# Performance work log

Hardware: AMD Instinct MI355X
Metric: run time of the kernel (lower is better)

The kernel has to match this reference:

```python
import jax, jax.numpy as jnp
import numpy as np

EPS = 1e-5

def _layer_norm(x, g, b):
    mu = jnp.mean(x, axis=-1, keepdims=True)
    var = jnp.mean(jnp.square(x - mu), axis=-1, keepdims=True)
    return (x - mu) * jax.lax.rsqrt(var + EPS) * g + b

def setup_inputs() -> dict:
    key = jax.random.key(0)
    ks = jax.random.split(key, 8)
    B, N, M = 4, 2048, 2048
    Dq, Dc = 512, 768
    H, Dh = 8, 64
    inner = H * Dh  # 512
    s = lambda d: 1.0 / np.sqrt(d)
    return {
        "x": jax.random.normal(ks[0], (B, N, Dq), jnp.float32),
        "cond": jax.random.normal(ks[1], (B, M, Dc), jnp.float32),
        "lnx_g": jnp.ones((Dq,), jnp.float32),
        "lnx_b": jnp.zeros((Dq,), jnp.float32),
        "lnc_g": jnp.ones((Dc,), jnp.float32),
        "lnc_b": jnp.zeros((Dc,), jnp.float32),
        "Wq": jax.random.normal(ks[2], (Dq, inner), jnp.float32) * s(Dq),
        "Wk": jax.random.normal(ks[3], (Dc, inner), jnp.float32) * s(Dc),
        "Wv": jax.random.normal(ks[4], (Dc, inner), jnp.float32) * s(Dc),
        "Wo": jax.random.normal(ks[5], (inner, Dq), jnp.float32) * s(inner),
        "bo": jnp.zeros((Dq,), jnp.float32),
        "lnf_g": jnp.ones((Dq,), jnp.float32),
        "lnf_b": jnp.zeros((Dq,), jnp.float32),
    }

def reference(x, cond, lnx_g, lnx_b, lnc_g, lnc_b, Wq, Wk, Wv, Wo, bo, lnf_g, lnf_b):
    H = 8
    B, N, _ = x.shape
    M = cond.shape[1]
    x_orig = x
    xn = _layer_norm(x, lnx_g, lnx_b)
    cn = _layer_norm(cond, lnc_g, lnc_b)
    q = (xn @ Wq).reshape(B, N, H, -1).transpose(0, 2, 1, 3)  # b h n d
    k = (cn @ Wk).reshape(B, M, H, -1).transpose(0, 2, 1, 3)  # b h m d
    v = (cn @ Wv).reshape(B, M, H, -1).transpose(0, 2, 1, 3)
    scale = q.shape[-1] ** -0.5
    sim = jnp.einsum('bhid,bhjd->bhij', q, k) * scale
    attn = jax.nn.softmax(sim, axis=-1)
    out = jnp.einsum('bhij,bhjd->bhid', attn, v)
    out = out.transpose(0, 2, 1, 3).reshape(B, N, -1)  # b n (h d)
    out = out @ Wo + bo
    out = out + x_orig  # residual=True
    return _layer_norm(out, lnf_g, lnf_b)
```

## Files before the change

### kernel.cpp

```cpp
#include <hip/hip_runtime.h>
#include <hip/hip_bf16.h>
#include <math.h>

#define BB 4
#define NN 2048
#define MM 2048
#define DQ 512
#define DC 768
#define NH 8
#define DH 64
#define INNER 512
#define KVS 1024

typedef short bf16x8 __attribute__((ext_vector_type(8)));
typedef float f32x4  __attribute__((ext_vector_type(4)));

__device__ inline short fbf(float f) {
    __hip_bfloat16 h = __float2bfloat16(f);
    return __builtin_bit_cast(short, h);
}

__device__ inline void gld16(const void* gptr, void* lds_uniform_base) {
    __builtin_amdgcn_global_load_lds(
        (const __attribute__((address_space(1))) void*)gptr,
        (__attribute__((address_space(3))) void*)lds_uniform_base, 16, 0, 0);
}

__global__ __launch_bounds__(256) void prep_k(
    const float* __restrict__ x, const float* __restrict__ cond,
    const float* __restrict__ gx, const float* __restrict__ bx_,
    const float* __restrict__ gc, const float* __restrict__ bc,
    short* __restrict__ xn, short* __restrict__ cn,
    const float* __restrict__ Wq, const float* __restrict__ Wk,
    const float* __restrict__ Wv, const float* __restrict__ Wo,
    short* __restrict__ Wqt, short* __restrict__ Wkvt, short* __restrict__ Wot)
{
    const int bxid = blockIdx.x;
    const int t = threadIdx.x;

    if (bxid < 16384) {
        const int which = bxid >> 13;
        const int row   = bxid & 8191;
        const float* in = which ? cond : x;
        const float* g  = which ? gc : gx;
        const float* bb = which ? bc : bx_;
        short* out      = which ? cn : xn;
        const int D     = which ? DC : DQ;

        const float* xr = in + (size_t)row * D;
        float s = 0.f, s2 = 0.f;
        for (int d = t; d < D; d += 256) {
            float v = xr[d];
            s += v; s2 += v * v;
        }
        __shared__ float red[2][4];
        #pragma unroll
        for (int off = 32; off; off >>= 1) {
            s  += __shfl_down(s,  off, 64);
            s2 += __shfl_down(s2, off, 64);
        }
        const int wave = t >> 6, lane = t & 63;
        if (lane == 0) { red[0][wave] = s; red[1][wave] = s2; }
        __syncthreads();
        if (t == 0) {
            float ts = red[0][0] + red[0][1] + red[0][2] + red[0][3];
            float t2 = red[1][0] + red[1][1] + red[1][2] + red[1][3];
            float mu = ts / (float)D;
            float var = t2 / (float)D - mu * mu;
            red[0][0] = mu;
            red[1][0] = rsqrtf(var + 1e-5f);
        }
        __syncthreads();
        const float mu = red[0][0], rstd = red[1][0];
        short* o = out + (size_t)row * D;
        for (int d = t; d < D; d += 256)
            o[d] = fbf((xr[d] - mu) * rstd * g[d] + bb[d]);
    } else {
        const int tb = bxid - 16384;
        const int y = tb >> 4;
        const int n0 = (tb & 15) * 32;
        const float* W; short* Wt; int K, k0;
        if (y < 16)      { W = Wq; Wt = Wqt;  K = DQ; k0 = y * 32; }
        else if (y < 40) { W = Wk; Wt = Wkvt; K = DC; k0 = (y - 16) * 32; }
        else if (y < 64) { W = Wv; Wt = Wkvt + (size_t)512 * DC; K = DC; k0 = (y - 40) * 32; }
        else             { W = Wo; Wt = Wot;  K = DQ; k0 = (y - 64) * 32; }

        __shared__ float tile[32][33];
        const int r = t >> 3, c4 = (t & 7) * 4;
        float4 vv = *(const float4*)&W[(size_t)(k0 + r) * 512 + n0 + c4];
        tile[c4 + 0][r] = vv.x; tile[c4 + 1][r] = vv.y;
        tile[c4 + 2][r] = vv.z; tile[c4 + 3][r] = vv.w;
        __syncthreads();
        short4 sv;
        sv.x = fbf(tile[r][c4 + 0]); sv.y = fbf(tile[r][c4 + 1]);
        sv.z = fbf(tile[r][c4 + 2]); sv.w = fbf(tile[r][c4 + 3]);
        *(short4*)&Wt[(size_t)(n0 + r) * K + k0 + c4] = sv;
    }
}

__global__ __launch_bounds__(256) void layernorm_res_f32(
    const short* __restrict__ ob, const float* __restrict__ x,
    const float* __restrict__ g, const float* __restrict__ b,
    float* __restrict__ out)
{
    const int row = blockIdx.x;
    const int t = threadIdx.x;
    const size_t base = (size_t)row * DQ;
    float v0, v1;
    {
        unsigned u0 = (unsigned)(unsigned short)ob[base + t];
        unsigned u1 = (unsigned)(unsigned short)ob[base + t + 256];
        v0 = __builtin_bit_cast(float, u0 << 16) + x[base + t];
        v1 = __builtin_bit_cast(float, u1 << 16) + x[base + t + 256];
    }
    float s = v0 + v1, s2 = v0 * v0 + v1 * v1;
    __shared__ float red[2][4];
    #pragma unroll
    for (int off = 32; off; off >>= 1) {
        s  += __shfl_down(s,  off, 64);
        s2 += __shfl_down(s2, off, 64);
    }
    const int wave = t >> 6, lane = t & 63;
    if (lane == 0) { red[0][wave] = s; red[1][wave] = s2; }
    __syncthreads();
    if (t == 0) {
        float ts = red[0][0] + red[0][1] + red[0][2] + red[0][3];
        float t2 = red[1][0] + red[1][1] + red[1][2] + red[1][3];
        float mu = ts / (float)DQ;
        float var = t2 / (float)DQ - mu * mu;
        red[0][0] = mu;
        red[1][0] = rsqrtf(var + 1e-5f);
    }
    __syncthreads();
    const float mu = red[0][0], rstd = red[1][0];
    out[base + t]       = (v0 - mu) * rstd * g[t]       + b[t];
    out[base + t + 256] = (v1 - mu) * rstd * g[t + 256] + b[t + 256];
}

#define GBK 32

__global__ __launch_bounds__(256) void qkv_gemm(
    const short* __restrict__ xn, const short* __restrict__ cn,
    const short* __restrict__ Wqt, const short* __restrict__ Wkvt,
    short* __restrict__ qb, short* __restrict__ kvb, float qsc)
{
    const short* A; const short* Bt; short* outp; int K, Nout, n0; float sc;
    if (blockIdx.x < 4) {
        A = xn; Bt = Wqt; outp = qb; K = DQ; Nout = 512;
        n0 = blockIdx.x * 128; sc = qsc;
    } else {
        A = cn; Bt = Wkvt; outp = kvb; K = DC; Nout = 1024;
        n0 = (blockIdx.x - 4) * 128; sc = 1.f;
    }
    __shared__ short As[128 * GBK];
    __shared__ short Bs[128 * GBK];
    const int t = threadIdx.x;
    const int w = t >> 6, lane = t & 63;
    const int quad = lane >> 4, l16 = lane & 15;
    const int m0 = blockIdx.y * 128;
    const int wm = (w >> 1) * 64, wn = (w & 1) * 64;

    f32x4 acc[4][4];
    #pragma unroll
    for (int i = 0; i < 4; ++i)
        #pragma unroll
        for (int j = 0; j < 4; ++j) acc[i][j] = (f32x4){0.f, 0.f, 0.f, 0.f};

    for (int kt = 0; kt < K; kt += GBK) {
        __syncthreads();
        #pragma unroll
        for (int i = 0; i < 2; ++i) {
            const int j = w * 2 + i;
            const int c = j * 64 + lane;
            gld16(&A[(size_t)(m0 + (c >> 2)) * K + kt + (c & 3) * 8],
                  (char*)As + j * 1024);
            gld16(&Bt[(size_t)(n0 + (c >> 2)) * K + kt + (c & 3) * 8],
                  (char*)Bs + j * 1024);
        }
        __syncthreads();

        bf16x8 af[4], bfr[4];
        #pragma unroll
        for (int mt = 0; mt < 4; ++mt)
            af[mt] = *(bf16x8*)&As[(wm + mt * 16 + l16) * GBK + quad * 8];
        #pragma unroll
        for (int nt = 0; nt < 4; ++nt)
            bfr[nt] = *(bf16x8*)&Bs[(wn + nt * 16 + l16) * GBK + quad * 8];
        #pragma unroll
        for (int mt = 0; mt < 4; ++mt)
            #pragma unroll
            for (int nt = 0; nt < 4; ++nt)
                acc[mt][nt] = __builtin_amdgcn_mfma_f32_16x16x32_bf16(
                    af[mt], bfr[nt], acc[mt][nt], 0, 0, 0);
    }

    #pragma unroll
    for (int mt = 0; mt < 4; ++mt)
        #pragma unroll
        for (int r = 0; r < 4; ++r) {
            const int m = m0 + wm + mt * 16 + quad * 4 + r;
            #pragma unroll
            for (int nt = 0; nt < 4; ++nt) {
                const int n = n0 + wn + nt * 16 + l16;
                outp[(size_t)m * Nout + n] = fbf(acc[mt][nt][r] * sc);
            }
        }
}

__global__ __launch_bounds__(256) void oproj_gemm(
    const short* __restrict__ A, const short* __restrict__ Bt,
    short* __restrict__ outb, const float* __restrict__ bias)
{
    const int K = INNER, Nout = INNER;
    __shared__ short As[128 * GBK];
    __shared__ short Bs[64 * GBK];
    const int t = threadIdx.x;
    const int w = t >> 6, lane = t & 63;
    const int quad = lane >> 4, l16 = lane & 15;
    const int m0 = blockIdx.y * 128, n0 = blockIdx.x * 64;
    const int wm = (w >> 1) * 64, wn = (w & 1) * 32;

    f32x4 acc[4][2];
    #pragma unroll
    for (int i = 0; i < 4; ++i)
        #pragma unroll
        for (int j = 0; j < 2; ++j) acc[i][j] = (f32x4){0.f, 0.f, 0.f, 0.f};

    for (int kt = 0; kt < K; kt += GBK) {
        __syncthreads();
        #pragma unroll
        for (int i = 0; i < 2; ++i) {
            const int j = w * 2 + i;
            const int c = j * 64 + lane;
            gld16(&A[(size_t)(m0 + (c >> 2)) * K + kt + (c & 3) * 8],
                  (char*)As + j * 1024);
        }
        {
            const int c = w * 64 + lane;
            gld16(&Bt[(size_t)(n0 + (c >> 2)) * K + kt + (c & 3) * 8],
                  (char*)Bs + w * 1024);
        }
        __syncthreads();

        bf16x8 af[4], bfr[2];
        #pragma unroll
        for (int mt = 0; mt < 4; ++mt)
            af[mt] = *(bf16x8*)&As[(wm + mt * 16 + l16) * GBK + quad * 8];
        #pragma unroll
        for (int nt = 0; nt < 2; ++nt)
            bfr[nt] = *(bf16x8*)&Bs[(wn + nt * 16 + l16) * GBK + quad * 8];
        #pragma unroll
        for (int mt = 0; mt < 4; ++mt)
            #pragma unroll
            for (int nt = 0; nt < 2; ++nt)
                acc[mt][nt] = __builtin_amdgcn_mfma_f32_16x16x32_bf16(
                    af[mt], bfr[nt], acc[mt][nt], 0, 0, 0);
    }

    #pragma unroll
    for (int mt = 0; mt < 4; ++mt)
        #pragma unroll
        for (int r = 0; r < 4; ++r) {
            const int m = m0 + wm + mt * 16 + quad * 4 + r;
            #pragma unroll
            for (int nt = 0; nt < 2; ++nt) {
                const int n = n0 + wn + nt * 16 + l16;
                outb[(size_t)m * Nout + n] = fbf(acc[mt][nt][r] + bias[n]);
            }
        }
}

#define QT 128
#define JT 64
#define KSTR 72
#define MH (MM / 2)
#define NIT (MH / JT)

__global__ __launch_bounds__(512) void attention_mfma(
    const short* __restrict__ q, const short* __restrict__ kv,
    short* __restrict__ o)
{
    const int b = blockIdx.z, h = blockIdx.y;
    const int i0 = blockIdx.x * QT;
    const int t = threadIdx.x;
    const int wave = t >> 6, lane = t & 63;
    const int w4 = wave & 3, hh = wave >> 2;
    const int quad = lane >> 4, l16 = lane & 15;

    __shared__ __align__(16) char smem[73728];
    typedef short KT[2][64][KSTR];
    KT* Ks = (KT*)smem;
    KT* Vt = (KT*)(smem + 36864);
    float (*Obuf)[32][68] = (float(*)[32][68])(smem);
    float (*Lbuf)[32]     = (float(*)[32])(smem + 34816);

    bf16x8 qf[2][2];
    #pragma unroll
    for (int it = 0; it < 2; ++it) {
        const int row = i0 + w4 * 32 + it * 16 + l16;
        const short* qp = &q[((size_t)(b * NN + row)) * INNER + h * DH];
        qf[it][0] = *(const bf16x8*)&qp[quad * 8];
        qf[it][1] = *(const bf16x8*)&qp[32 + quad * 8];
    }

    f32x4 Oa[2][4];
    f32x4 La[2];
    #pragma unroll
    for (int it = 0; it < 2; ++it) {
        La[it] = (f32x4){0.f, 0.f, 0.f, 0.f};
        #pragma unroll
        for (int dt = 0; dt < 4; ++dt) Oa[it][dt] = (f32x4){0.f, 0.f, 0.f, 0.f};
    }

    const bf16x8 ones8 = {(short)0x3F80, (short)0x3F80, (short)0x3F80, (short)0x3F80,
                          (short)0x3F80, (short)0x3F80, (short)0x3F80, (short)0x3F80};

    const int tt = t & 255, th = t >> 8;
    const int kjj = tt >> 3, kdq = (tt & 7) * 8;
    const int vjp = tt & 31, vd0 = (tt >> 5) * 8;

    const int jl0 = 2 * vjp;
    const int vcol = (jl0 >> 5) * 32 + (((jl0 >> 2) & 3) * 8)
                   + (((jl0 >> 4) & 1) * 4) + (jl0 & 3);

    const short* kp0 = kv + ((size_t)(b * MM + th * MH + kjj))      * KVS + h * DH + kdq;
    const short* kp1 = kv + ((size_t)(b * MM + th * MH + kjj + 32)) * KVS + h * DH + kdq;
    const short* vp0 = kv + ((size_t)(b * MM + th * MH + jl0))      * KVS + 512 + h * DH + vd0;
    const short* vp1 = vp0 + KVS;

    bf16x8 ka, kb2, va, vb;
    auto load = [&]() {
        ka  = *(const bf16x8*)kp0;
        kb2 = *(const bf16x8*)kp1;
        va  = *(const bf16x8*)vp0;
        vb  = *(const bf16x8*)vp1;
        kp0 += (size_t)JT * KVS; kp1 += (size_t)JT * KVS;
        vp0 += (size_t)JT * KVS; vp1 += (size_t)JT * KVS;
    };
    auto store = [&](int pb) {
        *(bf16x8*)&Ks[pb][th][kjj][kdq]      = ka;
        *(bf16x8*)&Ks[pb][th][kjj + 32][kdq] = kb2;
        #pragma unroll
        for (int i = 0; i < 8; ++i) {
            short2 pr; pr.x = va[i]; pr.y = vb[i];
            *(short2*)&Vt[pb][th][vd0 + i][vcol] = pr;
        }
    };

    load(); store(0);
    __syncthreads();

    for (int itr = 0; itr < NIT; ++itr) {
        const int p = itr & 1;
        const bool more = (itr + 1 < NIT);
        if (more) load();

        #pragma unroll
        for (int cc = 0; cc < 2; ++cc) {
            f32x4 Sc[2][2];
            #pragma unroll
            for (int jtl = 0; jtl < 2; ++jtl) {
                const int jt = cc * 2 + jtl;
                bf16x8 kf0 = *(bf16x8*)&Ks[p][hh][jt * 16 + l16][quad * 8];
                bf16x8 kf1 = *(bf16x8*)&Ks[p][hh][jt * 16 + l16][32 + quad * 8];
                #pragma unroll
                for (int it = 0; it < 2; ++it) {
                    f32x4 c = (f32x4){0.f, 0.f, 0.f, 0.f};
                    c = __builtin_amdgcn_mfma_f32_16x16x32_bf16(kf0, qf[it][0], c, 0, 0, 0);
                    c = __builtin_amdgcn_mfma_f32_16x16x32_bf16(kf1, qf[it][1], c, 0, 0, 0);
                    Sc[jtl][it] = c;
                }
            }

            bf16x8 p8[2];
            #pragma unroll
            for (int it = 0; it < 2; ++it) {
                const float e0 = exp2f(Sc[0][it][0]), e1 = exp2f(Sc[0][it][1]);
                const float e2 = exp2f(Sc[0][it][2]), e3 = exp2f(Sc[0][it][3]);
                const float f0 = exp2f(Sc[1][it][0]), f1 = exp2f(Sc[1][it][1]);
                const float f2 = exp2f(Sc[1][it][2]), f3 = exp2f(Sc[1][it][3]);
                uint4 pk;
                pk.x = __builtin_amdgcn_perm(__builtin_bit_cast(unsigned, e1),
                                             __builtin_bit_cast(unsigned, e0), 0x07060302u);
                pk.y = __builtin_amdgcn_perm(__builtin_bit_cast(unsigned, e3),
                                             __builtin_bit_cast(unsigned, e2), 0x07060302u);
                pk.z = __builtin_amdgcn_perm(__builtin_bit_cast(unsigned, f1),
                                             __builtin_bit_cast(unsigned, f0), 0x07060302u);
                pk.w = __builtin_amdgcn_perm(__builtin_bit_cast(unsigned, f3),
                                             __builtin_bit_cast(unsigned, f2), 0x07060302u);
                p8[it] = __builtin_bit_cast(bf16x8, pk);
            }

            #pragma unroll
            for (int dt = 0; dt < 4; ++dt) {
                bf16x8 vb8 = *(bf16x8*)&Vt[p][hh][dt * 16 + l16][cc * 32 + quad * 8];
                Oa[0][dt] = __builtin_amdgcn_mfma_f32_16x16x32_bf16(p8[0], vb8, Oa[0][dt], 0, 0, 0);
                Oa[1][dt] = __builtin_amdgcn_mfma_f32_16x16x32_bf16(p8[1], vb8, Oa[1][dt], 0, 0, 0);
            }
            La[0] = __builtin_amdgcn_mfma_f32_16x16x32_bf16(p8[0], ones8, La[0], 0, 0, 0);
            La[1] = __builtin_amdgcn_mfma_f32_16x16x32_bf16(p8[1], ones8, La[1], 0, 0, 0);
        }

        if (more) store(p ^ 1);
        __syncthreads();
    }

    if (wave >= 4) {
        #pragma unroll
        for (int it = 0; it < 2; ++it) {
            #pragma unroll
            for (int r = 0; r < 4; ++r) {
                const int qr = it * 16 + quad * 4 + r;
                #pragma unroll
                for (int dt = 0; dt < 4; ++dt)
                    Obuf[w4][qr][dt * 16 + l16] = Oa[it][dt][r];
                if (l16 == 0) Lbuf[w4][qr] = La[it][r];
            }
        }
    }
    __syncthreads();
    if (wave < 4) {
        #pragma unroll
        for (int it = 0; it < 2; ++it) {
            #pragma unroll
            for (int r = 0; r < 4; ++r) {
                const int qr = it * 16 + quad * 4 + r;
                const float ltot = La[it][r] + Lbuf[w4][qr];
                const float inv = 1.f / ltot;
                const int row = i0 + w4 * 32 + qr;
                #pragma unroll
                for (int dt = 0; dt < 4; ++dt) {
                    const float val = Oa[it][dt][r] + Obuf[w4][qr][dt * 16 + l16];
                    o[((size_t)(b * NN + row)) * INNER + h * DH + dt * 16 + l16] =
                        fbf(val * inv);
                }
            }
        }
    }
}

extern "C" void kernel_launch(void* const* d_in, const int* in_sizes, int n_in,
                              void* d_out, int out_size, void* d_ws, size_t ws_size,
                              hipStream_t stream)
{
    const float* x     = (const float*)d_in[0];
    const float* cond  = (const float*)d_in[1];
    const float* lnx_g = (const float*)d_in[2];
    const float* lnx_b = (const float*)d_in[3];
    const float* lnc_g = (const float*)d_in[4];
    const float* lnc_b = (const float*)d_in[5];
    const float* Wq    = (const float*)d_in[6];
    const float* Wk    = (const float*)d_in[7];
    const float* Wv    = (const float*)d_in[8];
    const float* Wo    = (const float*)d_in[9];
    const float* bo    = (const float*)d_in[10];
    const float* lnf_g = (const float*)d_in[11];
    const float* lnf_b = (const float*)d_in[12];
    float* out = (float*)d_out;
    char* ws = (char*)d_ws;

    const int R = BB * NN;

    short* xn_bf  = (short*)(ws);
    short* cn_bf  = (short*)(ws + (8u << 20));
    short* Wq_t   = (short*)(ws + (20u << 20));
    short* Wo_t   = (short*)(ws + (21u << 20));
    short* Wkv_t  = (short*)(ws + (22u << 20));
    short* qb     = (short*)(ws + (24u << 20));
    short* kvb    = (short*)(ws + (32u << 20));
    short* ab     = (short*)(ws + (48u << 20));
    short* ob     = (short*)(ws + (56u << 20));

    prep_k<<<17664, 256, 0, stream>>>(
        x, cond, lnx_g, lnx_b, lnc_g, lnc_b, xn_bf, cn_bf,
        Wq, Wk, Wv, Wo, Wq_t, Wkv_t, Wo_t);

    qkv_gemm<<<dim3(12, R / 128), 256, 0, stream>>>(
        xn_bf, cn_bf, Wq_t, Wkv_t, qb, kvb, 0.125f * 1.44269504089f);

    attention_mfma<<<dim3(NN / QT, NH, BB), 512, 0, stream>>>(qb, kvb, ab);

    oproj_gemm<<<dim3(INNER / 64, R / 128), 256, 0, stream>>>(ab, Wo_t, ob, bo);

    layernorm_res_f32<<<R, 256, 0, stream>>>(ob, x, lnf_g, lnf_b, out);
}
```

Baseline: 228.4 us.

## Split attention KV range across four wave groups with 1024-thread blocks

The attention kernel now uses 1024 threads per block, and the KV sequence is split into four quarters instead of two. Each group of four waves handles one quarter and partial outputs are combined through a two-step tree reduction in shared memory. To fit four K/V slices in the same LDS budget, the double buffer is removed, so each iteration needs an extra barrier and the prefetch is only held in registers. The aim is more parallel waves per query tile, at the cost of more synchronisation and less overlap between loads and compute.

Result: slower. 604.7 us (+164.7%).

```diff
diff --git a/kernel.cpp b/kernel.cpp
--- a/kernel.cpp
+++ b/kernel.cpp
@@ -273,10 +273,10 @@
 #define QT 128
 #define JT 64
 #define KSTR 72
-#define MH (MM / 2)
-#define NIT (MH / JT)
-
-__global__ __launch_bounds__(512) void attention_mfma(
+#define MQ (MM / 4)
+#define NIT (MQ / JT)
+
+__global__ __launch_bounds__(1024, 8) void attention_mfma(
     const short* __restrict__ q, const short* __restrict__ kv,
     short* __restrict__ o)
 {
@@ -284,15 +284,15 @@
     const int i0 = blockIdx.x * QT;
     const int t = threadIdx.x;
     const int wave = t >> 6, lane = t & 63;
-    const int w4 = wave & 3, hh = wave >> 2;
+    const int w4 = wave & 3;
+    const int hh = wave >> 2;
     const int quad = lane >> 4, l16 = lane & 15;
 
     __shared__ __align__(16) char smem[73728];
-    typedef short KT[2][64][KSTR];
-    KT* Ks = (KT*)smem;
-    KT* Vt = (KT*)(smem + 36864);
-    float (*Obuf)[32][68] = (float(*)[32][68])(smem);
-    float (*Lbuf)[32]     = (float(*)[32])(smem + 34816);
+    short (*Ks)[64][KSTR] = (short(*)[64][KSTR])(smem);
+    short (*Vt)[64][KSTR] = (short(*)[64][KSTR])(smem + 36864);
+    float (*Obuf)[4][32][68] = (float(*)[4][32][68])(smem);
+    float (*Lbuf)[4][32]     = (float(*)[4][32])(smem + 69632);
 
     bf16x8 qf[2][2];
     #pragma unroll
@@ -323,9 +323,9 @@
     const int vcol = (jl0 >> 5) * 32 + (((jl0 >> 2) & 3) * 8)
                    + (((jl0 >> 4) & 1) * 4) + (jl0 & 3);
 
-    const short* kp0 = kv + ((size_t)(b * MM + th * MH + kjj))      * KVS + h * DH + kdq;
-    const short* kp1 = kv + ((size_t)(b * MM + th * MH + kjj + 32)) * KVS + h * DH + kdq;
-    const short* vp0 = kv + ((size_t)(b * MM + th * MH + jl0))      * KVS + 512 + h * DH + vd0;
+    const short* kp0 = kv + ((size_t)(b * MM + th * MQ + kjj)) * KVS + h * DH + kdq;
+    const short* kp1 = kp0 + (size_t)32 * KVS;
+    const short* vp0 = kv + ((size_t)(b * MM + th * MQ + jl0)) * KVS + 512 + h * DH + vd0;
     const short* vp1 = vp0 + KVS;
 
     bf16x8 ka, kb2, va, vb;
@@ -337,21 +337,20 @@
         kp0 += (size_t)JT * KVS; kp1 += (size_t)JT * KVS;
         vp0 += (size_t)JT * KVS; vp1 += (size_t)JT * KVS;
     };
-    auto store = [&](int pb) {
-        *(bf16x8*)&Ks[pb][th][kjj][kdq]      = ka;
-        *(bf16x8*)&Ks[pb][th][kjj + 32][kdq] = kb2;
+    auto store = [&]() {
+        *(bf16x8*)&Ks[th][kjj][kdq]      = ka;
+        *(bf16x8*)&Ks[th][kjj + 32][kdq] = kb2;
         #pragma unroll
         for (int i = 0; i < 8; ++i) {
             short2 pr; pr.x = va[i]; pr.y = vb[i];
-            *(short2*)&Vt[pb][th][vd0 + i][vcol] = pr;
+            *(short2*)&Vt[th][vd0 + i][vcol] = pr;
         }
     };
 
-    load(); store(0);
+    load(); store();
     __syncthreads();
 
     for (int itr = 0; itr < NIT; ++itr) {
-        const int p = itr & 1;
         const bool more = (itr + 1 < NIT);
         if (more) load();
 
@@ -361,8 +360,8 @@
             #pragma unroll
             for (int jtl = 0; jtl < 2; ++jtl) {
                 const int jt = cc * 2 + jtl;
-                bf16x8 kf0 = *(bf16x8*)&Ks[p][hh][jt * 16 + l16][quad * 8];
-                bf16x8 kf1 = *(bf16x8*)&Ks[p][hh][jt * 16 + l16][32 + quad * 8];
+                bf16x8 kf0 = *(bf16x8*)&Ks[hh][jt * 16 + l16][quad * 8];
+                bf16x8 kf1 = *(bf16x8*)&Ks[hh][jt * 16 + l16][32 + quad * 8];
                 #pragma unroll
                 for (int it = 0; it < 2; ++it) {
                     f32x4 c = (f32x4){0.f, 0.f, 0.f, 0.f};
@@ -393,7 +392,7 @@
 
             #pragma unroll
             for (int dt = 0; dt < 4; ++dt) {
-                bf16x8 vb8 = *(bf16x8*)&Vt[p][hh][dt * 16 + l16][cc * 32 + quad * 8];
+                bf16x8 vb8 = *(bf16x8*)&Vt[hh][dt * 16 + l16][cc * 32 + quad * 8];
                 Oa[0][dt] = __builtin_amdgcn_mfma_f32_16x16x32_bf16(p8[0], vb8, Oa[0][dt], 0, 0, 0);
                 Oa[1][dt] = __builtin_amdgcn_mfma_f32_16x16x32_bf16(p8[1], vb8, Oa[1][dt], 0, 0, 0);
             }
@@ -401,41 +400,66 @@
             La[1] = __builtin_amdgcn_mfma_f32_16x16x32_bf16(p8[1], ones8, La[1], 0, 0, 0);
         }
 
-        if (more) store(p ^ 1);
-        __syncthreads();
-    }
-
-    if (wave >= 4) {
-        #pragma unroll
-        for (int it = 0; it < 2; ++it) {
+        __syncthreads();
+        if (more) { store(); __syncthreads(); }
+    }
+
+    const int pr_ = hh >> 1;
+    if (hh & 1) {
+        #pragma unroll
+        for (int it = 0; it < 2; ++it)
             #pragma unroll
             for (int r = 0; r < 4; ++r) {
                 const int qr = it * 16 + quad * 4 + r;
                 #pragma unroll
                 for (int dt = 0; dt < 4; ++dt)
-                    Obuf[w4][qr][dt * 16 + l16] = Oa[it][dt][r];
-                if (l16 == 0) Lbuf[w4][qr] = La[it][r];
-            }
-        }
+                    Obuf[pr_][w4][qr][dt * 16 + l16] = Oa[it][dt][r];
+                if (l16 == 0) Lbuf[pr_][w4][qr] = La[it][r];
+            }
     }
     __syncthreads();
-    if (wave < 4) {
-        #pragma unroll
-        for (int it = 0; it < 2; ++it) {
+    if (!(hh & 1)) {
+        #pragma unroll
+        for (int it = 0; it < 2; ++it)
             #pragma unroll
             for (int r = 0; r < 4; ++r) {
                 const int qr = it * 16 + quad * 4 + r;
-                const float ltot = La[it][r] + Lbuf[w4][qr];
+                La[it][r] += Lbuf[pr_][w4][qr];
+                #pragma unroll
+                for (int dt = 0; dt < 4; ++dt)
+                    Oa[it][dt][r] += Obuf[pr_][w4][qr][dt * 16 + l16];
+            }
+    }
+    __syncthreads();
+    if (hh == 2) {
+        #pragma unroll
+        for (int it = 0; it < 2; ++it)
+            #pragma unroll
+            for (int r = 0; r < 4; ++r) {
+                const int qr = it * 16 + quad * 4 + r;
+                #pragma unroll
+                for (int dt = 0; dt < 4; ++dt)
+                    Obuf[0][w4][qr][dt * 16 + l16] = Oa[it][dt][r];
+                if (l16 == 0) Lbuf[0][w4][qr] = La[it][r];
+            }
+    }
+    __syncthreads();
+    if (hh == 0) {
+        #pragma unroll
+        for (int it = 0; it < 2; ++it)
+            #pragma unroll
+            for (int r = 0; r < 4; ++r) {
+                const int qr = it * 16 + quad * 4 + r;
+                const float ltot = La[it][r] + Lbuf[0][w4][qr];
                 const float inv = 1.f / ltot;
                 const int row = i0 + w4 * 32 + qr;
                 #pragma unroll
                 for (int dt = 0; dt < 4; ++dt) {
-                    const float val = Oa[it][dt][r] + Obuf[w4][qr][dt * 16 + l16];
+                    const float val = Oa[it][dt][r] + Obuf[0][w4][qr][dt * 16 + l16];
                     o[((size_t)(b * NN + row)) * INNER + h * DH + dt * 16 + l16] =
                         fbf(val * inv);
                 }
             }
-        }
     }
 }
 
@@ -478,7 +502,7 @@
     qkv_gemm<<<dim3(12, R / 128), 256, 0, stream>>>(
         xn_bf, cn_bf, Wq_t, Wkv_t, qb, kvb, 0.125f * 1.44269504089f);
 
-    attention_mfma<<<dim3(NN / QT, NH, BB), 512, 0, stream>>>(qb, kvb, ab);
+    attention_mfma<<<dim3(NN / QT, NH, BB), 1024, 0, stream>>>(qb, kvb, ab);
 
     oproj_gemm<<<dim3(INNER / 64, R / 128), 256, 0, stream>>>(ab, Wo_t, ob, bo);
 
```
